# Kernel tuning notes

Hardware: AMD Instinct MI355X
Metric: run time of the kernel (lower is better)

The kernel has to match this reference:

```python
import jax, jax.numpy as jnp
import numpy as np

N_QUBITS = 10
N_QLAYERS = 2
EMBED = 1024
B, S = 16, 1024
DIM = 2 ** N_QUBITS


def _apply_rx(state, theta, w, n):
    # state: [N, 2^n] complex; RX(theta) on wire w (wire 0 = most significant bit)
    nb = state.shape[0]
    left, right = 2 ** w, 2 ** (n - 1 - w)
    psi = state.reshape(nb, left, 2, right)
    t = jnp.asarray(theta, jnp.float32) * 0.5
    c, s = jnp.cos(t), jnp.sin(t)
    if c.ndim == 1:  # per-sample angles
        c, s = c[:, None, None], s[:, None, None]
    a0, a1 = psi[:, :, 0, :], psi[:, :, 1, :]
    n0 = c * a0 - 1j * s * a1
    n1 = -1j * s * a0 + c * a1
    return jnp.stack([n0, n1], axis=2).reshape(nb, -1)


def _apply_cnot(state, c, t, n):
    # CNOT with control wire c, target wire t
    psi = state.reshape((-1,) + (2,) * n)
    ctrl_ax, tgt_ax = c + 1, t + 1
    psi0, psi1 = jnp.split(psi, 2, axis=ctrl_ax)
    psi1 = jnp.flip(psi1, axis=tgt_ax)
    return jnp.concatenate([psi0, psi1], axis=ctrl_ax).reshape(state.shape)


def setup_inputs() -> dict:
    key = jax.random.key(0)
    ks = jax.random.split(key, 6)
    s1 = 1.0 / np.sqrt(EMBED)
    s2 = 1.0 / np.sqrt(N_QUBITS)
    return {
        "x": jax.random.normal(ks[0], (B, S, EMBED), jnp.float32),
        "W1": jax.random.uniform(ks[1], (N_QUBITS, EMBED), jnp.float32, -s1, s1),
        "b1": jax.random.uniform(ks[2], (N_QUBITS,), jnp.float32, -s1, s1),
        "qweights": jax.random.uniform(ks[3], (N_QLAYERS, N_QUBITS), jnp.float32, 0.0, 2.0 * np.pi),
        "W2": jax.random.uniform(ks[4], (EMBED, N_QUBITS), jnp.float32, -s2, s2),
        "b2": jax.random.uniform(ks[5], (EMBED,), jnp.float32, -s2, s2),
    }


def reference(x, W1, b1, qweights, W2, b2):
    n = N_QUBITS
    # linear_1
    ang = (jnp.einsum('bse,qe->bsq', x, W1) + b1).reshape(-1, n)  # [N, n]
    N = ang.shape[0]
    # |0...0> batched state vector
    state = jnp.zeros((N, DIM), jnp.complex64).at[:, 0].set(1.0)
    # AngleEmbedding: RX(ang[:, w]) on each wire
    for w in range(n):
        state = _apply_rx(state, ang[:, w], w, n)
    # BasicEntanglerLayers: RX rotations + CNOT ring per layer
    for l in range(N_QLAYERS):
        for w in range(n):
            state = _apply_rx(state, qweights[l, w], w, n)
        if n == 2:
            state = _apply_cnot(state, 0, 1, n)
        elif n > 2:
            for i in range(n):
                state = _apply_cnot(state, i, (i + 1) % n, n)
    # <Z_w> = sum_idx probs[idx] * (1 - 2*bit_w(idx))
    probs = jnp.real(state * jnp.conj(state))  # [N, 2^n]
    idx = jnp.arange(DIM)
    bits = (idx[:, None] >> (n - 1 - jnp.arange(n))[None, :]) & 1
    signs = (1 - 2 * bits).astype(jnp.float32)  # [2^n, n]
    ev = (probs @ signs).reshape(x.shape[0], x.shape[1], n)  # [B, S, n]
    # linear_2
    return jnp.einsum('bsq,eq->bse', ev, W2) + b2
```

## Files before the change

kernel.cpp:

```cpp
#include <hip/hip_runtime.h>

#define NQ 10
#define EMBED 1024
#define ROWS_PER_BLOCK 32
#define BLOCK 512


constexpr int kPop(int x) { int c = 0; for (int i = 0; i < 10; ++i) c += (x >> i) & 1; return c; }

constexpr int sigma_map(int a) {
    int b = 0;
    for (int i = 0; i < 9; ++i) b |= (((a >> i) & 1) ^ ((a >> (i + 1)) & 1)) << i;
    b |= (((a >> 9) & 1) ^ ((a >> 0) & 1) ^ ((a >> 1) & 1)) << 9;
    return b;
}

#define MAXT 40
struct Terms {
    int nt[NQ];
    int vm[NQ];
    int um[NQ];
    unsigned short tm[NQ][MAXT];
    unsigned short sm[NQ][MAXT];
    float sg[NQ][MAXT];
};

constexpr Terms gen_terms() {
    Terms t{};
    int inv_e[NQ] = {};
    for (int a = 0; a < 1024; ++a) {
        const int s = sigma_map(a);
        for (int q = 0; q < NQ; ++q) if (s == (1 << q)) inv_e[q] = a;
    }
    for (int q = 0; q < NQ; ++q) {
        const int u = inv_e[q];
        int v = 0;
        for (int w = 0; w < NQ; ++w) if ((u >> w) & 1) v ^= inv_e[w];
        t.um[q] = u; t.vm[q] = v;
        int n = 0;
        int S = 0;
        while (true) {
            int T = (((S >> 0) ^ (S >> 9)) & 1)
                  | ((((S >> 0) ^ (S >> 1) ^ (S >> 9)) & 1) << 1);
            for (int j = 2; j < 10; ++j) T |= ((((S >> (j - 1)) ^ (S >> j)) & 1) << j);
            if ((T & ~v) == 0) {
                const int p = kPop(T) + kPop(S);
                if (!(p & 1)) {
                    t.tm[q][n] = (unsigned short)T;
                    t.sm[q][n] = (unsigned short)S;
                    t.sg[q][n] = (p & 2) ? -1.f : 1.f;
                    ++n;
                }
            }
            if (S == u) break;
            S = (S - u) & u;
        }
        t.nt[q] = n;
    }
    return t;
}

constexpr Terms TT = gen_terms();

extern "C" __global__ __launch_bounds__(BLOCK, 4)
void ffq_kernel(const float* __restrict__ x, const float* __restrict__ W1,
                const float* __restrict__ b1, const float* __restrict__ qw,
                const float* __restrict__ W2, const float* __restrict__ b2,
                float* __restrict__ out)
{
    __shared__ float sW1[NQ * EMBED];
    __shared__ float sCA[ROWS_PER_BLOCK][NQ];
    __shared__ float sSA[ROWS_PER_BLOCK][NQ];
    __shared__ float sEV[ROWS_PER_BLOCK][NQ];

    const int tid  = threadIdx.x;
    const int lane = tid & 63;
    const int wv   = tid >> 6;
    const int o    = lane & 31;
    const int g    = lane >> 5;
    const int block0 = blockIdx.x * ROWS_PER_BLOCK;

    const int e4 = tid & 255;
    float w2f[40];
    {
        const float4* w2v = (const float4*)(W2 + e4 * 40);
        #pragma unroll
        for (int i = 0; i < 10; ++i) {
            float4 v = w2v[i];
            w2f[4*i+0] = v.x; w2f[4*i+1] = v.y; w2f[4*i+2] = v.z; w2f[4*i+3] = v.w;
        }
    }
    const float4 b2v = ((const float4*)b2)[e4];

    float b1r[NQ], qw0[NQ];
    #pragma unroll
    for (int w = 0; w < NQ; ++w) { qw0[w] = qw[w]; b1r[w] = b1[w]; }

    {
        const float4* src = (const float4*)W1;
        float4* dst = (float4*)sW1;
        #pragma unroll
        for (int i = 0; i < 5; ++i) dst[tid + BLOCK * i] = src[tid + BLOCK * i];
    }
    __syncthreads();

    {
        const int rloc0 = wv * 4 + g * 2;
        float acc0[NQ], acc1[NQ];
        #pragma unroll
        for (int q = 0; q < NQ; ++q) { acc0[q] = 0.f; acc1[q] = 0.f; }

        const float4* xr0 = (const float4*)(x + (size_t)(block0 + rloc0) * EMBED);
        const float4* xr1 = (const float4*)(x + (size_t)(block0 + rloc0 + 1) * EMBED);
        const float4* w1v = (const float4*)sW1;
        #pragma unroll
        for (int k = 0; k < 8; ++k) {
            const float4 xv0 = xr0[k * 32 + o];
            const float4 xv1 = xr1[k * 32 + o];
            #pragma unroll
            for (int q = 0; q < NQ; ++q) {
                const float4 wv4 = w1v[q * 256 + k * 32 + o];
                acc0[q] = fmaf(xv0.x, wv4.x, acc0[q]);
                acc0[q] = fmaf(xv0.y, wv4.y, acc0[q]);
                acc0[q] = fmaf(xv0.z, wv4.z, acc0[q]);
                acc0[q] = fmaf(xv0.w, wv4.w, acc0[q]);
                acc1[q] = fmaf(xv1.x, wv4.x, acc1[q]);
                acc1[q] = fmaf(xv1.y, wv4.y, acc1[q]);
                acc1[q] = fmaf(xv1.z, wv4.z, acc1[q]);
                acc1[q] = fmaf(xv1.w, wv4.w, acc1[q]);
            }
        }
        #pragma unroll
        for (int m = 1; m < 32; m <<= 1) {
            #pragma unroll
            for (int q = 0; q < NQ; ++q) {
                acc0[q] += __shfl_xor(acc0[q], m, 64);
                acc1[q] += __shfl_xor(acc1[q], m, 64);
            }
        }
        if (o == 0) {
            #pragma unroll
            for (int w = 0; w < NQ; ++w) {
                const float A0 = acc0[w] + b1r[w] + qw0[w];
                const float A1 = acc1[w] + b1r[w] + qw0[w];
                sCA[rloc0][w]     = __cosf(A0);
                sSA[rloc0][w]     = __sinf(A0);
                sCA[rloc0 + 1][w] = __cosf(A1);
                sSA[rloc0 + 1][w] = __sinf(A1);
            }
        }
    }

    __syncthreads();

    if (lane < ROWS_PER_BLOCK) {
        const int row = lane;
        float ca[NQ], sa[NQ], cb[NQ], sb[NQ];
        #pragma unroll
        for (int w = 0; w < NQ; ++w) {
            ca[w] = sCA[row][w];
            sa[w] = sSA[row][w];
            const float B = qw[NQ + w];
            cb[w] = __cosf(B); sb[w] = __sinf(B);
        }
        #define EVQ(QC) do {                                                      \
            float ev = 0.f;                                                       \
            _Pragma("unroll")                                                     \
            for (int k = 0; k < TT.nt[QC]; ++k) {                                 \
                float P = TT.sg[QC][k];                                           \
                _Pragma("unroll")                                                 \
                for (int w = 0; w < NQ; ++w) {                                    \
                    if ((TT.vm[QC] >> w) & 1) P *= ((TT.tm[QC][k] >> w) & 1) ? sa[w] : ca[w]; \
                    if ((TT.um[QC] >> w) & 1) P *= ((TT.sm[QC][k] >> w) & 1) ? sb[w] : cb[w]; \
                }                                                                 \
                ev += P;                                                          \
            }                                                                     \
            sEV[row][QC] = ev;                                                    \
        } while (0)
        switch (wv) {
            case 0: EVQ(0); break;
            case 1: EVQ(9); break;
            case 2: EVQ(7); break;
            case 3: EVQ(8); break;
            case 4: EVQ(5); EVQ(6); break;
            case 5: EVQ(3); EVQ(4); break;
            case 6: EVQ(1); EVQ(2); break;
            default: break;
        }
        #undef EVQ
    }

    __syncthreads();

    const int r0 = (tid >> 8) * 16;
    #pragma unroll
    for (int r = 0; r < 16; ++r) {
        const int rr = r0 + r;
        float evr[NQ];
        #pragma unroll
        for (int q = 0; q < NQ; ++q) evr[q] = sEV[rr][q];
        float o0 = b2v.x, o1 = b2v.y, o2 = b2v.z, o3 = b2v.w;
        #pragma unroll
        for (int q = 0; q < NQ; ++q) {
            o0 = fmaf(evr[q], w2f[ 0 + q], o0);
            o1 = fmaf(evr[q], w2f[10 + q], o1);
            o2 = fmaf(evr[q], w2f[20 + q], o2);
            o3 = fmaf(evr[q], w2f[30 + q], o3);
        }
        float4 ov = {o0, o1, o2, o3};
        ((float4*)(out + (size_t)(block0 + rr) * EMBED))[e4] = ov;
    }
}

extern "C" void kernel_launch(void* const* d_in, const int* in_sizes, int n_in,
                              void* d_out, int out_size, void* d_ws, size_t ws_size,
                              hipStream_t stream) {
    (void)in_sizes; (void)n_in; (void)d_ws; (void)ws_size; (void)out_size;
    const float* x  = (const float*)d_in[0];
    const float* W1 = (const float*)d_in[1];
    const float* b1 = (const float*)d_in[2];
    const float* qw = (const float*)d_in[3];
    const float* W2 = (const float*)d_in[4];
    const float* b2 = (const float*)d_in[5];
    float* out = (float*)d_out;

    const int total_rows = 16 * 1024;
    dim3 grid(total_rows / ROWS_PER_BLOCK);
    ffq_kernel<<<grid, BLOCK, 0, stream>>>(x, W1, b1, qw, W2, b2, out);
}
```

Baseline: 32.34 us.

## Split fused kernel into EV kernel and output projection kernel via scratch in output

Splits the single fused kernel into two launches. The first computes the angles and expectation values, spreading the EV term evaluation across all waves with lanes taking row-by-qubit work through shuffles instead of shared-memory staging. It then writes the EVs into the first 10 floats of each output row. The second kernel reads those EVs back and computes the W2 projection with smaller blocks and more of them. This removes a block-level barrier and idle waves in the fused version, at the cost of a second launch, extra global round-trip traffic and a read-after-write dependency on the output buffer.

```diff
diff --git a/kernel.cpp b/kernel.cpp
--- a/kernel.cpp
+++ b/kernel.cpp
@@ -2,8 +2,6 @@
 
 #define NQ 10
 #define EMBED 1024
-#define ROWS_PER_BLOCK 32
-#define BLOCK 512
 
 
 constexpr int kPop(int x) { int c = 0; for (int i = 0; i < 10; ++i) c += (x >> i) & 1; return c; }
@@ -62,107 +60,84 @@
 
 constexpr Terms TT = gen_terms();
 
-extern "C" __global__ __launch_bounds__(BLOCK, 4)
-void ffq_kernel(const float* __restrict__ x, const float* __restrict__ W1,
-                const float* __restrict__ b1, const float* __restrict__ qw,
-                const float* __restrict__ W2, const float* __restrict__ b2,
-                float* __restrict__ out)
+extern "C" __global__ __launch_bounds__(512, 4)
+void ffq_ev_kernel(const float* __restrict__ x, const float* __restrict__ W1,
+                   const float* __restrict__ b1, const float* __restrict__ qw,
+                   float* __restrict__ out)
 {
     __shared__ float sW1[NQ * EMBED];
-    __shared__ float sCA[ROWS_PER_BLOCK][NQ];
-    __shared__ float sSA[ROWS_PER_BLOCK][NQ];
-    __shared__ float sEV[ROWS_PER_BLOCK][NQ];
 
     const int tid  = threadIdx.x;
     const int lane = tid & 63;
     const int wv   = tid >> 6;
     const int o    = lane & 31;
     const int g    = lane >> 5;
-    const int block0 = blockIdx.x * ROWS_PER_BLOCK;
-
-    const int e4 = tid & 255;
-    float w2f[40];
-    {
-        const float4* w2v = (const float4*)(W2 + e4 * 40);
-        #pragma unroll
-        for (int i = 0; i < 10; ++i) {
-            float4 v = w2v[i];
-            w2f[4*i+0] = v.x; w2f[4*i+1] = v.y; w2f[4*i+2] = v.z; w2f[4*i+3] = v.w;
-        }
-    }
-    const float4 b2v = ((const float4*)b2)[e4];
-
-    float b1r[NQ], qw0[NQ];
-    #pragma unroll
-    for (int w = 0; w < NQ; ++w) { qw0[w] = qw[w]; b1r[w] = b1[w]; }
+    const int block0 = blockIdx.x * 32;
 
     {
         const float4* src = (const float4*)W1;
         float4* dst = (float4*)sW1;
         #pragma unroll
-        for (int i = 0; i < 5; ++i) dst[tid + BLOCK * i] = src[tid + BLOCK * i];
-    }
+        for (int i = 0; i < 5; ++i) dst[tid + 512 * i] = src[tid + 512 * i];
+    }
+
+    float b1r[NQ], qw0[NQ];
+    #pragma unroll
+    for (int w = 0; w < NQ; ++w) { qw0[w] = qw[w]; b1r[w] = b1[w]; }
+
     __syncthreads();
 
-    {
-        const int rloc0 = wv * 4 + g * 2;
-        float acc0[NQ], acc1[NQ];
-        #pragma unroll
-        for (int q = 0; q < NQ; ++q) { acc0[q] = 0.f; acc1[q] = 0.f; }
-
-        const float4* xr0 = (const float4*)(x + (size_t)(block0 + rloc0) * EMBED);
-        const float4* xr1 = (const float4*)(x + (size_t)(block0 + rloc0 + 1) * EMBED);
-        const float4* w1v = (const float4*)sW1;
-        #pragma unroll
-        for (int k = 0; k < 8; ++k) {
-            const float4 xv0 = xr0[k * 32 + o];
-            const float4 xv1 = xr1[k * 32 + o];
-            #pragma unroll
-            for (int q = 0; q < NQ; ++q) {
-                const float4 wv4 = w1v[q * 256 + k * 32 + o];
-                acc0[q] = fmaf(xv0.x, wv4.x, acc0[q]);
-                acc0[q] = fmaf(xv0.y, wv4.y, acc0[q]);
-                acc0[q] = fmaf(xv0.z, wv4.z, acc0[q]);
-                acc0[q] = fmaf(xv0.w, wv4.w, acc0[q]);
-                acc1[q] = fmaf(xv1.x, wv4.x, acc1[q]);
-                acc1[q] = fmaf(xv1.y, wv4.y, acc1[q]);
-                acc1[q] = fmaf(xv1.z, wv4.z, acc1[q]);
-                acc1[q] = fmaf(xv1.w, wv4.w, acc1[q]);
-            }
-        }
-        #pragma unroll
-        for (int m = 1; m < 32; m <<= 1) {
-            #pragma unroll
-            for (int q = 0; q < NQ; ++q) {
-                acc0[q] += __shfl_xor(acc0[q], m, 64);
-                acc1[q] += __shfl_xor(acc1[q], m, 64);
-            }
-        }
-        if (o == 0) {
-            #pragma unroll
-            for (int w = 0; w < NQ; ++w) {
-                const float A0 = acc0[w] + b1r[w] + qw0[w];
-                const float A1 = acc1[w] + b1r[w] + qw0[w];
-                sCA[rloc0][w]     = __cosf(A0);
-                sSA[rloc0][w]     = __sinf(A0);
-                sCA[rloc0 + 1][w] = __cosf(A1);
-                sSA[rloc0 + 1][w] = __sinf(A1);
-            }
-        }
-    }
-
-    __syncthreads();
-
-    if (lane < ROWS_PER_BLOCK) {
-        const int row = lane;
-        float ca[NQ], sa[NQ], cb[NQ], sb[NQ];
-        #pragma unroll
-        for (int w = 0; w < NQ; ++w) {
-            ca[w] = sCA[row][w];
-            sa[w] = sSA[row][w];
-            const float B = qw[NQ + w];
-            cb[w] = __cosf(B); sb[w] = __sinf(B);
-        }
+    const int rloc0 = wv * 4 + g * 2;
+    float acc0[NQ], acc1[NQ];
+    #pragma unroll
+    for (int q = 0; q < NQ; ++q) { acc0[q] = 0.f; acc1[q] = 0.f; }
+
+    const float4* xr0 = (const float4*)(x + (size_t)(block0 + rloc0) * EMBED);
+    const float4* xr1 = (const float4*)(x + (size_t)(block0 + rloc0 + 1) * EMBED);
+    const float4* w1v = (const float4*)sW1;
+    #pragma unroll
+    for (int k = 0; k < 8; ++k) {
+        const float4 xv0 = xr0[k * 32 + o];
+        const float4 xv1 = xr1[k * 32 + o];
+        #pragma unroll
+        for (int q = 0; q < NQ; ++q) {
+            const float4 wv4 = w1v[q * 256 + k * 32 + o];
+            acc0[q] = fmaf(xv0.x, wv4.x, acc0[q]);
+            acc0[q] = fmaf(xv0.y, wv4.y, acc0[q]);
+            acc0[q] = fmaf(xv0.z, wv4.z, acc0[q]);
+            acc0[q] = fmaf(xv0.w, wv4.w, acc0[q]);
+            acc1[q] = fmaf(xv1.x, wv4.x, acc1[q]);
+            acc1[q] = fmaf(xv1.y, wv4.y, acc1[q]);
+            acc1[q] = fmaf(xv1.z, wv4.z, acc1[q]);
+            acc1[q] = fmaf(xv1.w, wv4.w, acc1[q]);
+        }
+    }
+    #pragma unroll
+    for (int m = 1; m < 32; m <<= 1) {
+        #pragma unroll
+        for (int q = 0; q < NQ; ++q) {
+            acc0[q] += __shfl_xor(acc0[q], m, 64);
+            acc1[q] += __shfl_xor(acc1[q], m, 64);
+        }
+    }
+
+    const int r   = lane & 3;
+    const int grp = lane >> 2;
+    const int srcl = (r & 2) ? 32 : 0;
+
+    float ca[NQ], sa[NQ], cb[NQ], sb[NQ];
+    #pragma unroll
+    for (int w = 0; w < NQ; ++w) {
+        const float a0 = __shfl(acc0[w], srcl, 64);
+        const float a1 = __shfl(acc1[w], srcl, 64);
+        const float A  = ((r & 1) ? a1 : a0) + b1r[w] + qw0[w];
+        ca[w] = __cosf(A); sa[w] = __sinf(A);
+        const float B = qw[NQ + w];
+        cb[w] = __cosf(B); sb[w] = __sinf(B);
+    }
+
+    if (grp < 7) {
+        float* orow = out + (size_t)(block0 + wv * 4 + r) * EMBED;
         #define EVQ(QC) do {                                                      \
             float ev = 0.f;                                                       \
             _Pragma("unroll")                                                     \
@@ -175,40 +150,61 @@
                 }                                                                 \
                 ev += P;                                                          \
             }                                                                     \
-            sEV[row][QC] = ev;                                                    \
+            orow[QC] = ev;                                                        \
         } while (0)
-        switch (wv) {
+        switch (grp) {
             case 0: EVQ(0); break;
             case 1: EVQ(9); break;
             case 2: EVQ(7); break;
             case 3: EVQ(8); break;
             case 4: EVQ(5); EVQ(6); break;
             case 5: EVQ(3); EVQ(4); break;
-            case 6: EVQ(1); EVQ(2); break;
-            default: break;
+            default: EVQ(1); EVQ(2); break;
         }
         #undef EVQ
     }
-
+}
+
+extern "C" __global__ __launch_bounds__(256, 4)
+void ffq_out_kernel(const float* __restrict__ W2, const float* __restrict__ b2,
+                    float* __restrict__ out)
+{
+    __shared__ float sev[80];
+
+    const int tid = threadIdx.x;
+    const int r0  = blockIdx.x * 8;
+
+    float w2f[40];
+    {
+        const float4* w2v = (const float4*)(W2 + tid * 40);
+        #pragma unroll
+        for (int i = 0; i < 10; ++i) {
+            float4 v = w2v[i];
+            w2f[4*i+0] = v.x; w2f[4*i+1] = v.y; w2f[4*i+2] = v.z; w2f[4*i+3] = v.w;
+        }
+    }
+    const float4 b2v = ((const float4*)b2)[tid];
+
+    if (tid < 80) {
+        const int rr = tid / 10;
+        const int qq = tid - rr * 10;
+        sev[tid] = out[(size_t)(r0 + rr) * EMBED + qq];
+    }
     __syncthreads();
 
-    const int r0 = (tid >> 8) * 16;
-    #pragma unroll
-    for (int r = 0; r < 16; ++r) {
-        const int rr = r0 + r;
-        float evr[NQ];
-        #pragma unroll
-        for (int q = 0; q < NQ; ++q) evr[q] = sEV[rr][q];
+    #pragma unroll
+    for (int rr = 0; rr < 8; ++rr) {
         float o0 = b2v.x, o1 = b2v.y, o2 = b2v.z, o3 = b2v.w;
         #pragma unroll
         for (int q = 0; q < NQ; ++q) {
-            o0 = fmaf(evr[q], w2f[ 0 + q], o0);
-            o1 = fmaf(evr[q], w2f[10 + q], o1);
-            o2 = fmaf(evr[q], w2f[20 + q], o2);
-            o3 = fmaf(evr[q], w2f[30 + q], o3);
+            const float e = sev[rr * 10 + q];
+            o0 = fmaf(e, w2f[ 0 + q], o0);
+            o1 = fmaf(e, w2f[10 + q], o1);
+            o2 = fmaf(e, w2f[20 + q], o2);
+            o3 = fmaf(e, w2f[30 + q], o3);
         }
         float4 ov = {o0, o1, o2, o3};
-        ((float4*)(out + (size_t)(block0 + rr) * EMBED))[e4] = ov;
+        ((float4*)(out + (size_t)(r0 + rr) * EMBED))[tid] = ov;
     }
 }
 
@@ -224,7 +220,6 @@
     const float* b2 = (const float*)d_in[5];
     float* out = (float*)d_out;
 
-    const int total_rows = 16 * 1024;
-    dim3 grid(total_rows / ROWS_PER_BLOCK);
-    ffq_kernel<<<grid, BLOCK, 0, stream>>>(x, W1, b1, qw, W2, b2, out);
-}
+    ffq_ev_kernel<<<dim3(512), 512, 0, stream>>>(x, W1, b1, qw, out);
+    ffq_out_kernel<<<dim3(2048), 256, 0, stream>>>(W2, b2, out);
+}
```

New measurement: 47.35 us. 46.4% more time.

## Prefetch x rows up front, DPP row reductions, defer W2 loads, pad shared arrays

Applied to the files above, without the earlier changes.

Issues all eight float4 loads of each x row before the FMA loop so global latency overlaps, and splits the W1 shared-memory reads into two groups of five. Replaces the shfl_xor butterfly reduction with DPP row operations, so only lane 16 or 17 holds each row's result and the cos/sin work is split between those two lanes. Moves the W2/b2 register loads after the first stage, folds b1 and qw into one array, and pads the small shared arrays to stride 11. The added live registers from prefetching could raise register pressure under the launch bounds.

```diff
diff --git a/kernel.cpp b/kernel.cpp
--- a/kernel.cpp
+++ b/kernel.cpp
@@ -62,6 +62,20 @@
 
 constexpr Terms TT = gen_terms();
 
+template <int CTRL, int RM>
+__device__ __forceinline__ float dppadd(float v) {
+    const int s = __builtin_amdgcn_update_dpp(0, __float_as_int(v), CTRL, RM, 0xF, true);
+    return v + __int_as_float(s);
+}
+__device__ __forceinline__ float red32(float v) {
+    v = dppadd<0xB1,  0xF>(v);
+    v = dppadd<0x4E,  0xF>(v);
+    v = dppadd<0x141, 0xF>(v);
+    v = dppadd<0x140, 0xF>(v);
+    v = dppadd<0x142, 0xA>(v);
+    return v;
+}
+
 extern "C" __global__ __launch_bounds__(BLOCK, 4)
 void ffq_kernel(const float* __restrict__ x, const float* __restrict__ W1,
                 const float* __restrict__ b1, const float* __restrict__ qw,
@@ -69,9 +83,9 @@
                 float* __restrict__ out)
 {
     __shared__ float sW1[NQ * EMBED];
-    __shared__ float sCA[ROWS_PER_BLOCK][NQ];
-    __shared__ float sSA[ROWS_PER_BLOCK][NQ];
-    __shared__ float sEV[ROWS_PER_BLOCK][NQ];
+    __shared__ float sCA[ROWS_PER_BLOCK][11];
+    __shared__ float sSA[ROWS_PER_BLOCK][11];
+    __shared__ float sEVv[ROWS_PER_BLOCK][11];
 
     const int tid  = threadIdx.x;
     const int lane = tid & 63;
@@ -80,6 +94,90 @@
     const int g    = lane >> 5;
     const int block0 = blockIdx.x * ROWS_PER_BLOCK;
 
+    {
+        const float4* src = (const float4*)W1;
+        float4* dst = (float4*)sW1;
+        #pragma unroll
+        for (int i = 0; i < 5; ++i) dst[tid + BLOCK * i] = src[tid + BLOCK * i];
+    }
+
+    float b1q[NQ];
+    #pragma unroll
+    for (int w = 0; w < NQ; ++w) b1q[w] = b1[w] + qw[w];
+
+    __syncthreads();
+
+    {
+        const int rloc0 = wv * 4 + g * 2;
+        const float4* xr0 = (const float4*)(x + (size_t)(block0 + rloc0) * EMBED);
+        const float4* xr1 = (const float4*)(x + (size_t)(block0 + rloc0 + 1) * EMBED);
+
+        float4 xv0[8], xv1[8];
+        #pragma unroll
+        for (int k = 0; k < 8; ++k) xv0[k] = xr0[k * 32 + o];
+        #pragma unroll
+        for (int k = 0; k < 8; ++k) xv1[k] = xr1[k * 32 + o];
+
+        float acc0[NQ], acc1[NQ];
+        #pragma unroll
+        for (int q = 0; q < NQ; ++q) { acc0[q] = 0.f; acc1[q] = 0.f; }
+
+        const float4* w1v = (const float4*)sW1;
+        #pragma unroll
+        for (int k = 0; k < 8; ++k) {
+            float4 wA[5];
+            #pragma unroll
+            for (int q = 0; q < 5; ++q) wA[q] = w1v[q * 256 + k * 32 + o];
+            #pragma unroll
+            for (int q = 0; q < 5; ++q) {
+                acc0[q] = fmaf(xv0[k].x, wA[q].x, acc0[q]);
+                acc0[q] = fmaf(xv0[k].y, wA[q].y, acc0[q]);
+                acc0[q] = fmaf(xv0[k].z, wA[q].z, acc0[q]);
+                acc0[q] = fmaf(xv0[k].w, wA[q].w, acc0[q]);
+                acc1[q] = fmaf(xv1[k].x, wA[q].x, acc1[q]);
+                acc1[q] = fmaf(xv1[k].y, wA[q].y, acc1[q]);
+                acc1[q] = fmaf(xv1[k].z, wA[q].z, acc1[q]);
+                acc1[q] = fmaf(xv1[k].w, wA[q].w, acc1[q]);
+            }
+            float4 wB[5];
+            #pragma unroll
+            for (int q = 0; q < 5; ++q) wB[q] = w1v[(5 + q) * 256 + k * 32 + o];
+            #pragma unroll
+            for (int q = 0; q < 5; ++q) {
+                acc0[5+q] = fmaf(xv0[k].x, wB[q].x, acc0[5+q]);
+                acc0[5+q] = fmaf(xv0[k].y, wB[q].y, acc0[5+q]);
+                acc0[5+q] = fmaf(xv0[k].z, wB[q].z, acc0[5+q]);
+                acc0[5+q] = fmaf(xv0[k].w, wB[q].w, acc0[5+q]);
+                acc1[5+q] = fmaf(xv1[k].x, wB[q].x, acc1[5+q]);
+                acc1[5+q] = fmaf(xv1[k].y, wB[q].y, acc1[5+q]);
+                acc1[5+q] = fmaf(xv1[k].z, wB[q].z, acc1[5+q]);
+                acc1[5+q] = fmaf(xv1[k].w, wB[q].w, acc1[5+q]);
+            }
+        }
+
+        #pragma unroll
+        for (int q = 0; q < NQ; ++q) {
+            acc0[q] = red32(acc0[q]);
+            acc1[q] = red32(acc1[q]);
+        }
+
+        if (o == 16) {
+            #pragma unroll
+            for (int w = 0; w < NQ; ++w) {
+                const float A = acc0[w] + b1q[w];
+                sCA[rloc0][w] = __cosf(A);
+                sSA[rloc0][w] = __sinf(A);
+            }
+        } else if (o == 17) {
+            #pragma unroll
+            for (int w = 0; w < NQ; ++w) {
+                const float A = acc1[w] + b1q[w];
+                sCA[rloc0 + 1][w] = __cosf(A);
+                sSA[rloc0 + 1][w] = __sinf(A);
+            }
+        }
+    }
+
     const int e4 = tid & 255;
     float w2f[40];
     {
@@ -91,65 +189,6 @@
         }
     }
     const float4 b2v = ((const float4*)b2)[e4];
-
-    float b1r[NQ], qw0[NQ];
-    #pragma unroll
-    for (int w = 0; w < NQ; ++w) { qw0[w] = qw[w]; b1r[w] = b1[w]; }
-
-    {
-        const float4* src = (const float4*)W1;
-        float4* dst = (float4*)sW1;
-        #pragma unroll
-        for (int i = 0; i < 5; ++i) dst[tid + BLOCK * i] = src[tid + BLOCK * i];
-    }
-    __syncthreads();
-
-    {
-        const int rloc0 = wv * 4 + g * 2;
-        float acc0[NQ], acc1[NQ];
-        #pragma unroll
-        for (int q = 0; q < NQ; ++q) { acc0[q] = 0.f; acc1[q] = 0.f; }
-
-        const float4* xr0 = (const float4*)(x + (size_t)(block0 + rloc0) * EMBED);
-        const float4* xr1 = (const float4*)(x + (size_t)(block0 + rloc0 + 1) * EMBED);
-        const float4* w1v = (const float4*)sW1;
-        #pragma unroll
-        for (int k = 0; k < 8; ++k) {
-            const float4 xv0 = xr0[k * 32 + o];
-            const float4 xv1 = xr1[k * 32 + o];
-            #pragma unroll
-            for (int q = 0; q < NQ; ++q) {
-                const float4 wv4 = w1v[q * 256 + k * 32 + o];
-                acc0[q] = fmaf(xv0.x, wv4.x, acc0[q]);
-                acc0[q] = fmaf(xv0.y, wv4.y, acc0[q]);
-                acc0[q] = fmaf(xv0.z, wv4.z, acc0[q]);
-                acc0[q] = fmaf(xv0.w, wv4.w, acc0[q]);
-                acc1[q] = fmaf(xv1.x, wv4.x, acc1[q]);
-                acc1[q] = fmaf(xv1.y, wv4.y, acc1[q]);
-                acc1[q] = fmaf(xv1.z, wv4.z, acc1[q]);
-                acc1[q] = fmaf(xv1.w, wv4.w, acc1[q]);
-            }
-        }
-        #pragma unroll
-        for (int m = 1; m < 32; m <<= 1) {
-            #pragma unroll
-            for (int q = 0; q < NQ; ++q) {
-                acc0[q] += __shfl_xor(acc0[q], m, 64);
-                acc1[q] += __shfl_xor(acc1[q], m, 64);
-            }
-        }
-        if (o == 0) {
-            #pragma unroll
-            for (int w = 0; w < NQ; ++w) {
-                const float A0 = acc0[w] + b1r[w] + qw0[w];
-                const float A1 = acc1[w] + b1r[w] + qw0[w];
-                sCA[rloc0][w]     = __cosf(A0);
-                sSA[rloc0][w]     = __sinf(A0);
-                sCA[rloc0 + 1][w] = __cosf(A1);
-                sSA[rloc0 + 1][w] = __sinf(A1);
-            }
-        }
-    }
 
     __syncthreads();
 
@@ -175,7 +214,7 @@
                 }                                                                 \
                 ev += P;                                                          \
             }                                                                     \
-            sEV[row][QC] = ev;                                                    \
+            sEVv[row][QC] = ev;                                                   \
         } while (0)
         switch (wv) {
             case 0: EVQ(0); break;
@@ -198,7 +237,7 @@
         const int rr = r0 + r;
         float evr[NQ];
         #pragma unroll
-        for (int q = 0; q < NQ; ++q) evr[q] = sEV[rr][q];
+        for (int q = 0; q < NQ; ++q) evr[q] = sEVv[rr][q];
         float o0 = b2v.x, o1 = b2v.y, o2 = b2v.z, o3 = b2v.w;
         #pragma unroll
         for (int q = 0; q < NQ; ++q) {
```

After: 28.27 us. 12.6% less time.
